# Optimization experiments

Measured on AMD Instinct MI355X. Metric: run time of the kernel, lower is better.

## Reference

```python
import jax, jax.numpy as jnp
import numpy as np

BLOCK_SIZE = 5
DROP_RATE = 0.5


def setup_inputs() -> dict:
    key = jax.random.key(0)
    k1, k2 = jax.random.split(key)
    B, C, H, W = 64, 128, 56, 56
    bs = BLOCK_SIZE
    x = jax.random.normal(k1, (B, C, H, W), dtype=jnp.float32)
    # uniform noise used to realize the Bernoulli(gamma) sample deterministically
    u = jax.random.uniform(k2, (B, C, H - bs + 1, W - bs + 1), dtype=jnp.float32)
    return {"x": x, "u": u, "num_batches_tracked": 1}


def reference(x, u, num_batches_tracked):
    bs = BLOCK_SIZE
    B, C, H, W = x.shape
    # keep-rate schedule (num_batches_tracked is a Python int => static)
    keep_rate = max(1.0 - DROP_RATE / 20000.0 * num_batches_tracked, 1.0 - DROP_RATE)
    gamma = (1.0 - keep_rate) / bs ** 2 * W ** 2 / (W - bs + 1) ** 2
    # Bernoulli(gamma) sample on the valid (H-bs+1, W-bs+1) grid
    mask = (u < gamma).astype(x.dtype)
    # The original scatters 1s at offsets 0..bs-1 around each sampled point into
    # a padded (H, W) mask. That is exactly a bs x bs max-pool dilation with
    # (bs-1, bs-1) zero padding on each spatial side, producing an (H, W) output.
    dilated = jax.lax.reduce_window(
        mask, 0.0, jax.lax.max,
        window_dimensions=(1, 1, bs, bs),
        window_strides=(1, 1, 1, 1),
        padding=((0, 0), (0, 0), (bs - 1, bs - 1), (bs - 1, bs - 1)),
    )
    block_mask = 1.0 - dilated  # (B, C, H, W)
    countM = block_mask.size
    count_ones = block_mask.sum()
    dind = (countM / count_ones) * block_mask
    return x * dind
```

## Files before the change

kernel.cpp:

```cpp
#include <hip/hip_runtime.h>

namespace {
constexpr int BSZ = 5;
constexpr int Bn = 64, Cn = 128, Hn = 56, Wn = 56;
constexpr int HU = Hn - BSZ + 1;
constexpr int WU = Wn - BSZ + 1;
constexpr long long NX = (long long)Bn * Cn * Hn * Wn;
constexpr long long NU = (long long)Bn * Cn * HU * WU;
constexpr int PLANE_U = HU * WU;
constexpr int PLANE_X = Hn * Wn;
constexpr int MAXH = 8192;

constexpr int NU4 = (int)(NU / 4);
constexpr int NX4 = (int)(NX / 4);
constexpr int SCAN_BLOCKS = NU4 / 256;
constexpr int MUL_BLOCKS = NX4 / 256;

struct Ctl {
  unsigned int nhits;
  unsigned int pad0;
  float scale;
  unsigned int hits[MAXH];
};
}

__global__ __launch_bounds__(256) void k_scan(const float4* __restrict__ u4,
                                              const int* __restrict__ nbt,
                                              Ctl* ctl) {
  double kr = 1.0 - 0.5 / 20000.0 * (double)nbt[0];
  if (kr < 0.5) kr = 0.5;
  double gd = (1.0 - kr) / (double)(BSZ * BSZ) * (double)(Wn * Wn) /
              (double)((Wn - BSZ + 1) * (Wn - BSZ + 1));
  const float g = (float)gd;

  const int i = blockIdx.x * 256 + threadIdx.x;
  float4 v = u4[i];
  if (v.x < g || v.y < g || v.z < g || v.w < g) {
    unsigned int base = (unsigned int)(4 * i);
    if (v.x < g) { unsigned int p = atomicAdd(&ctl->nhits, 1u); if (p < MAXH) ctl->hits[p] = base + 0u; }
    if (v.y < g) { unsigned int p = atomicAdd(&ctl->nhits, 1u); if (p < MAXH) ctl->hits[p] = base + 1u; }
    if (v.z < g) { unsigned int p = atomicAdd(&ctl->nhits, 1u); if (p < MAXH) ctl->hits[p] = base + 2u; }
    if (v.w < g) { unsigned int p = atomicAdd(&ctl->nhits, 1u); if (p < MAXH) ctl->hits[p] = base + 3u; }
  }
}

__global__ void k_count(Ctl* ctl) {
  __shared__ unsigned int s_total;
  if (threadIdx.x == 0) s_total = 0u;
  __syncthreads();
  const int n = (int)min(ctl->nhits, (unsigned int)MAXH);
  unsigned int local = 0;
  for (int t = threadIdx.x; t < n * 25; t += blockDim.x) {
    const int hi = t / 25;
    const int cell = t - hi * 25;
    const unsigned int e = ctl->hits[hi];
    const int plane = (int)(e / PLANE_U);
    const int rem = (int)(e - (unsigned int)plane * PLANE_U);
    const int i = rem / WU;
    const int j = rem - i * WU;
    const int hh = i + cell / 5;
    const int ww = j + cell % 5;
    bool covered = false;
    for (int p = 0; p < hi; ++p) {
      const unsigned int e2 = ctl->hits[p];
      const int pl2 = (int)(e2 / PLANE_U);
      if (pl2 != plane) continue;
      const int rem2 = (int)(e2 - (unsigned int)pl2 * PLANE_U);
      const int i2 = rem2 / WU;
      const int j2 = rem2 - i2 * WU;
      if (hh >= i2 && hh <= i2 + 4 && ww >= j2 && ww <= j2 + 4) { covered = true; break; }
    }
    if (!covered) local++;
  }
  if (local) atomicAdd(&s_total, local);
  __syncthreads();
  if (threadIdx.x == 0) {
    double count_ones = (double)NX - (double)s_total;
    ctl->scale = (float)((double)NX / count_ones);
  }
}

__global__ __launch_bounds__(256) void k_mul(const float4* __restrict__ x4,
                                             float4* __restrict__ o4,
                                             const Ctl* __restrict__ ctl) {
  const float s = ctl->scale;
  const int i = blockIdx.x * 256 + threadIdx.x;
  float4 v = x4[i];
  v.x *= s; v.y *= s; v.z *= s; v.w *= s;
  o4[i] = v;
}

__global__ void k_zero(float* __restrict__ out, const Ctl* __restrict__ ctl) {
  const int n = (int)min(ctl->nhits, (unsigned int)MAXH);
  const int total = n * 25;
  const int stride = gridDim.x * blockDim.x;
  for (int t = blockIdx.x * blockDim.x + threadIdx.x; t < total; t += stride) {
    const int hi = t / 25;
    const int cell = t - hi * 25;
    const unsigned int e = ctl->hits[hi];
    const int plane = (int)(e / PLANE_U);
    const int rem = (int)(e - (unsigned int)plane * PLANE_U);
    const int i = rem / WU;
    const int j = rem - i * WU;
    const int hh = i + cell / 5;
    const int ww = j + cell % 5;
    out[(long long)plane * PLANE_X + (long long)hh * Wn + ww] = 0.0f;
  }
}

extern "C" void kernel_launch(void* const* d_in, const int* in_sizes, int n_in,
                              void* d_out, int out_size, void* d_ws, size_t ws_size,
                              hipStream_t stream) {
  const float* x = (const float*)d_in[0];
  const float* u = (const float*)d_in[1];
  const int* nbt = (const int*)d_in[2];
  float* out = (float*)d_out;
  Ctl* ctl = (Ctl*)d_ws;

  hipMemsetAsync(ctl, 0, 8, stream);
  k_scan<<<SCAN_BLOCKS, 256, 0, stream>>>((const float4*)u, nbt, ctl);
  k_count<<<1, 256, 0, stream>>>(ctl);
  k_mul<<<MUL_BLOCKS, 256, 0, stream>>>((const float4*)x, (float4*)out, ctl);
  k_zero<<<16, 256, 0, stream>>>(out, ctl);
}
```

Measured before the change: 69.73 us.

## Fuse block zeroing into scale kernel and process four float4s per thread

Removes the separate k_zero launch by having k_mul check, per block, whether any recorded hit falls in its planes and, if so, zero the covered elements in registers before storing. Scan and mul kernels now handle four float4 per thread with a quarter of the blocks. This saves one kernel launch and the scattered zero writes. In exchange, every block scans the whole hit list, and blocks whose planes contain a hit then loop over all hits serially.

```diff
diff --git a/kernel.cpp b/kernel.cpp
--- a/kernel.cpp
+++ b/kernel.cpp
@@ -3,18 +3,15 @@
 namespace {
 constexpr int BSZ = 5;
 constexpr int Bn = 64, Cn = 128, Hn = 56, Wn = 56;
-constexpr int HU = Hn - BSZ + 1;
-constexpr int WU = Wn - BSZ + 1;
 constexpr long long NX = (long long)Bn * Cn * Hn * Wn;
-constexpr long long NU = (long long)Bn * Cn * HU * WU;
-constexpr int PLANE_U = HU * WU;
-constexpr int PLANE_X = Hn * Wn;
+constexpr long long NU = (long long)Bn * Cn * 52 * 52;
+constexpr int PLANE_U = 52 * 52;
+constexpr int PLANE_X4 = 784;
 constexpr int MAXH = 8192;
-
 constexpr int NU4 = (int)(NU / 4);
 constexpr int NX4 = (int)(NX / 4);
-constexpr int SCAN_BLOCKS = NU4 / 256;
-constexpr int MUL_BLOCKS = NX4 / 256;
+constexpr int SCAN_BLOCKS = NU4 / 1024;
+constexpr int MUL_BLOCKS  = NX4 / 1024;
 
 struct Ctl {
   unsigned int nhits;
@@ -22,26 +19,46 @@
   float scale;
   unsigned int hits[MAXH];
 };
+
+__device__ __forceinline__ void record_hits(float4 v, int idx4, float g, Ctl* ctl) {
+  if (v.x < g || v.y < g || v.z < g || v.w < g) {
+    unsigned int b = (unsigned int)(4 * idx4);
+    if (v.x < g) { unsigned int p = atomicAdd(&ctl->nhits, 1u); if (p < MAXH) ctl->hits[p] = b + 0u; }
+    if (v.y < g) { unsigned int p = atomicAdd(&ctl->nhits, 1u); if (p < MAXH) ctl->hits[p] = b + 1u; }
+    if (v.z < g) { unsigned int p = atomicAdd(&ctl->nhits, 1u); if (p < MAXH) ctl->hits[p] = b + 2u; }
+    if (v.w < g) { unsigned int p = atomicAdd(&ctl->nhits, 1u); if (p < MAXH) ctl->hits[p] = b + 3u; }
+  }
+}
+
+__device__ __forceinline__ void apply_hit(float4& a, int p, int row, int c0,
+                                          int hp, int hi, int hj) {
+  if (hp == p && row >= hi && row <= hi + 4) {
+    if (c0 + 0 >= hj && c0 + 0 <= hj + 4) a.x = 0.0f;
+    if (c0 + 1 >= hj && c0 + 1 <= hj + 4) a.y = 0.0f;
+    if (c0 + 2 >= hj && c0 + 2 <= hj + 4) a.z = 0.0f;
+    if (c0 + 3 >= hj && c0 + 3 <= hj + 4) a.w = 0.0f;
+  }
+}
 }
 
 __global__ __launch_bounds__(256) void k_scan(const float4* __restrict__ u4,
                                               const int* __restrict__ nbt,
-                                              Ctl* ctl) {
+                                              Ctl* __restrict__ ctl) {
   double kr = 1.0 - 0.5 / 20000.0 * (double)nbt[0];
   if (kr < 0.5) kr = 0.5;
   double gd = (1.0 - kr) / (double)(BSZ * BSZ) * (double)(Wn * Wn) /
               (double)((Wn - BSZ + 1) * (Wn - BSZ + 1));
   const float g = (float)gd;
 
-  const int i = blockIdx.x * 256 + threadIdx.x;
-  float4 v = u4[i];
-  if (v.x < g || v.y < g || v.z < g || v.w < g) {
-    unsigned int base = (unsigned int)(4 * i);
-    if (v.x < g) { unsigned int p = atomicAdd(&ctl->nhits, 1u); if (p < MAXH) ctl->hits[p] = base + 0u; }
-    if (v.y < g) { unsigned int p = atomicAdd(&ctl->nhits, 1u); if (p < MAXH) ctl->hits[p] = base + 1u; }
-    if (v.z < g) { unsigned int p = atomicAdd(&ctl->nhits, 1u); if (p < MAXH) ctl->hits[p] = base + 2u; }
-    if (v.w < g) { unsigned int p = atomicAdd(&ctl->nhits, 1u); if (p < MAXH) ctl->hits[p] = base + 3u; }
-  }
+  const int base = blockIdx.x * 1024 + threadIdx.x;
+  float4 v0 = u4[base];
+  float4 v1 = u4[base + 256];
+  float4 v2 = u4[base + 512];
+  float4 v3 = u4[base + 768];
+  record_hits(v0, base, g, ctl);
+  record_hits(v1, base + 256, g, ctl);
+  record_hits(v2, base + 512, g, ctl);
+  record_hits(v3, base + 768, g, ctl);
 }
 
 __global__ void k_count(Ctl* ctl) {
@@ -56,8 +73,8 @@
     const unsigned int e = ctl->hits[hi];
     const int plane = (int)(e / PLANE_U);
     const int rem = (int)(e - (unsigned int)plane * PLANE_U);
-    const int i = rem / WU;
-    const int j = rem - i * WU;
+    const int i = rem / 52;
+    const int j = rem - i * 52;
     const int hh = i + cell / 5;
     const int ww = j + cell % 5;
     bool covered = false;
@@ -66,8 +83,8 @@
       const int pl2 = (int)(e2 / PLANE_U);
       if (pl2 != plane) continue;
       const int rem2 = (int)(e2 - (unsigned int)pl2 * PLANE_U);
-      const int i2 = rem2 / WU;
-      const int j2 = rem2 - i2 * WU;
+      const int i2 = rem2 / 52;
+      const int j2 = rem2 - i2 * 52;
       if (hh >= i2 && hh <= i2 + 4 && ww >= j2 && ww <= j2 + 4) { covered = true; break; }
     }
     if (!covered) local++;
@@ -83,29 +100,56 @@
 __global__ __launch_bounds__(256) void k_mul(const float4* __restrict__ x4,
                                              float4* __restrict__ o4,
                                              const Ctl* __restrict__ ctl) {
+  const int blockStart = blockIdx.x * 1024;
+  const int base = blockStart + threadIdx.x;
+  float4 a0 = x4[base];
+  float4 a1 = x4[base + 256];
+  float4 a2 = x4[base + 512];
+  float4 a3 = x4[base + 768];
+
   const float s = ctl->scale;
-  const int i = blockIdx.x * 256 + threadIdx.x;
-  float4 v = x4[i];
-  v.x *= s; v.y *= s; v.z *= s; v.w *= s;
-  o4[i] = v;
-}
+  a0.x *= s; a0.y *= s; a0.z *= s; a0.w *= s;
+  a1.x *= s; a1.y *= s; a1.z *= s; a1.w *= s;
+  a2.x *= s; a2.y *= s; a2.z *= s; a2.w *= s;
+  a3.x *= s; a3.y *= s; a3.z *= s; a3.w *= s;
 
-__global__ void k_zero(float* __restrict__ out, const Ctl* __restrict__ ctl) {
   const int n = (int)min(ctl->nhits, (unsigned int)MAXH);
-  const int total = n * 25;
-  const int stride = gridDim.x * blockDim.x;
-  for (int t = blockIdx.x * blockDim.x + threadIdx.x; t < total; t += stride) {
-    const int hi = t / 25;
-    const int cell = t - hi * 25;
-    const unsigned int e = ctl->hits[hi];
-    const int plane = (int)(e / PLANE_U);
-    const int rem = (int)(e - (unsigned int)plane * PLANE_U);
-    const int i = rem / WU;
-    const int j = rem - i * WU;
-    const int hh = i + cell / 5;
-    const int ww = j + cell % 5;
-    out[(long long)plane * PLANE_X + (long long)hh * Wn + ww] = 0.0f;
+  const int pmin = blockStart / PLANE_X4;
+  const int pmax = (blockStart + 1023) / PLANE_X4;
+  bool any = false;
+  for (int h0 = 0; h0 < n; h0 += 64) {
+    const int h = h0 + (int)(threadIdx.x & 63);
+    bool mine = false;
+    if (h < n) {
+      const int hp = (int)(ctl->hits[h] / (unsigned int)PLANE_U);
+      mine = (hp >= pmin && hp <= pmax);
+    }
+    if (__any(mine)) { any = true; break; }
   }
+  if (any) {
+    const int f1 = base + 256, f2 = base + 512, f3 = base + 768;
+    const int p0 = base / PLANE_X4, p1 = f1 / PLANE_X4, p2 = f2 / PLANE_X4, p3 = f3 / PLANE_X4;
+    const int r0 = base - p0 * PLANE_X4, r1 = f1 - p1 * PLANE_X4,
+              r2 = f2 - p2 * PLANE_X4, r3 = f3 - p3 * PLANE_X4;
+    const int row0 = r0 / 14, row1 = r1 / 14, row2 = r2 / 14, row3 = r3 / 14;
+    const int c00 = (r0 - row0 * 14) * 4, c01 = (r1 - row1 * 14) * 4,
+              c02 = (r2 - row2 * 14) * 4, c03 = (r3 - row3 * 14) * 4;
+    for (int h = 0; h < n; ++h) {
+      const unsigned int e = ctl->hits[h];
+      const int hp = (int)(e / (unsigned int)PLANE_U);
+      const int rem = (int)(e - (unsigned int)hp * PLANE_U);
+      const int hi = rem / 52;
+      const int hj = rem - hi * 52;
+      apply_hit(a0, p0, row0, c00, hp, hi, hj);
+      apply_hit(a1, p1, row1, c01, hp, hi, hj);
+      apply_hit(a2, p2, row2, c02, hp, hi, hj);
+      apply_hit(a3, p3, row3, c03, hp, hi, hj);
+    }
+  }
+  o4[base] = a0;
+  o4[base + 256] = a1;
+  o4[base + 512] = a2;
+  o4[base + 768] = a3;
 }
 
 extern "C" void kernel_launch(void* const* d_in, const int* in_sizes, int n_in,
@@ -117,9 +161,8 @@
   float* out = (float*)d_out;
   Ctl* ctl = (Ctl*)d_ws;
 
-  hipMemsetAsync(ctl, 0, 8, stream);
+  hipMemsetAsync(&ctl->nhits, 0, sizeof(unsigned int), stream);
   k_scan<<<SCAN_BLOCKS, 256, 0, stream>>>((const float4*)u, nbt, ctl);
   k_count<<<1, 256, 0, stream>>>(ctl);
   k_mul<<<MUL_BLOCKS, 256, 0, stream>>>((const float4*)x, (float4*)out, ctl);
-  k_zero<<<16, 256, 0, stream>>>(out, ctl);
 }
```

Measured after the change: 70.11 us. Within noise of the previous version (+0.5%).

## Fuse scan, count, scale and mask into one persistent kernel with grid barrier

Applied to the files above, without the earlier changes.

Replaces the four separate kernels with one kernel where each block owns 8 planes: it scans its slice of u for hits into shared memory, counts uncovered cells locally, and adds that count to a global counter. It then prefetches part of x into registers, waits on a global atomic barrier for all blocks, computes the scale, and writes the output with masking applied inline. This removes extra launches and the separate zeroing pass. The barrier assumes all 1024 blocks are co-resident and falls back to a slow full rescan in every block if it times out.

```diff
diff --git a/kernel.cpp b/kernel.cpp
--- a/kernel.cpp
+++ b/kernel.cpp
@@ -1,125 +1,211 @@
 #include <hip/hip_runtime.h>
+
+typedef float f32x4 __attribute__((ext_vector_type(4)));
 
 namespace {
 constexpr int BSZ = 5;
-constexpr int Bn = 64, Cn = 128, Hn = 56, Wn = 56;
-constexpr int HU = Hn - BSZ + 1;
-constexpr int WU = Wn - BSZ + 1;
-constexpr long long NX = (long long)Bn * Cn * Hn * Wn;
-constexpr long long NU = (long long)Bn * Cn * HU * WU;
-constexpr int PLANE_U = HU * WU;
-constexpr int PLANE_X = Hn * Wn;
-constexpr int MAXH = 8192;
-
-constexpr int NU4 = (int)(NU / 4);
-constexpr int NX4 = (int)(NX / 4);
-constexpr int SCAN_BLOCKS = NU4 / 256;
-constexpr int MUL_BLOCKS = NX4 / 256;
-
-struct Ctl {
-  unsigned int nhits;
-  unsigned int pad0;
-  float scale;
-  unsigned int hits[MAXH];
-};
-}
-
-__global__ __launch_bounds__(256) void k_scan(const float4* __restrict__ u4,
+constexpr int Wn = 56;
+constexpr long long NX = 25690112;
+constexpr int NBLK = 1024;
+constexpr int T = 512;
+constexpr int PPB = 8;
+constexpr int U_PLANE = 2704;
+constexpr int UB = PPB * U_PLANE / 4;
+constexpr int XB = PPB * 3136 / 4;
+constexpr int PF = 10;
+constexpr int MAXL = 64;
+constexpr int NU4 = 5537792;
+
+__device__ __forceinline__ void mask_f4(f32x4& a, int k, const unsigned short* hits, int n) {
+  const int pl = k / 784;
+  const int rem4 = k - pl * 784;
+  const int row = rem4 / 14;
+  const int c0 = (rem4 - row * 14) * 4;
+  for (int h = 0; h < n; ++h) {
+    const int lin = hits[h];
+    const int hp = lin / U_PLANE;
+    if (hp != pl) continue;
+    const int hrem = lin - hp * U_PLANE;
+    const int hi = hrem / 52;
+    const int hj = hrem - hi * 52;
+    if (row >= hi && row <= hi + 4) {
+      if (c0 + 0 >= hj && c0 + 0 <= hj + 4) a.x = 0.0f;
+      if (c0 + 1 >= hj && c0 + 1 <= hj + 4) a.y = 0.0f;
+      if (c0 + 2 >= hj && c0 + 2 <= hj + 4) a.z = 0.0f;
+      if (c0 + 3 >= hj && c0 + 3 <= hj + 4) a.w = 0.0f;
+    }
+  }
+}
+}
+
+__global__ __launch_bounds__(T, 8) void k_all(const f32x4* __restrict__ u4,
+                                              const f32x4* __restrict__ x4,
+                                              f32x4* __restrict__ o4,
                                               const int* __restrict__ nbt,
-                                              Ctl* ctl) {
+                                              unsigned int* __restrict__ ws) {
+  const int tid = threadIdx.x;
+  const int blk = blockIdx.x;
+
   double kr = 1.0 - 0.5 / 20000.0 * (double)nbt[0];
   if (kr < 0.5) kr = 0.5;
   double gd = (1.0 - kr) / (double)(BSZ * BSZ) * (double)(Wn * Wn) /
               (double)((Wn - BSZ + 1) * (Wn - BSZ + 1));
   const float g = (float)gd;
 
-  const int i = blockIdx.x * 256 + threadIdx.x;
-  float4 v = u4[i];
-  if (v.x < g || v.y < g || v.z < g || v.w < g) {
-    unsigned int base = (unsigned int)(4 * i);
-    if (v.x < g) { unsigned int p = atomicAdd(&ctl->nhits, 1u); if (p < MAXH) ctl->hits[p] = base + 0u; }
-    if (v.y < g) { unsigned int p = atomicAdd(&ctl->nhits, 1u); if (p < MAXH) ctl->hits[p] = base + 1u; }
-    if (v.z < g) { unsigned int p = atomicAdd(&ctl->nhits, 1u); if (p < MAXH) ctl->hits[p] = base + 2u; }
-    if (v.w < g) { unsigned int p = atomicAdd(&ctl->nhits, 1u); if (p < MAXH) ctl->hits[p] = base + 3u; }
-  }
-}
-
-__global__ void k_count(Ctl* ctl) {
-  __shared__ unsigned int s_total;
-  if (threadIdx.x == 0) s_total = 0u;
-  __syncthreads();
-  const int n = (int)min(ctl->nhits, (unsigned int)MAXH);
-  unsigned int local = 0;
-  for (int t = threadIdx.x; t < n * 25; t += blockDim.x) {
-    const int hi = t / 25;
-    const int cell = t - hi * 25;
-    const unsigned int e = ctl->hits[hi];
-    const int plane = (int)(e / PLANE_U);
-    const int rem = (int)(e - (unsigned int)plane * PLANE_U);
-    const int i = rem / WU;
-    const int j = rem - i * WU;
-    const int hh = i + cell / 5;
-    const int ww = j + cell % 5;
-    bool covered = false;
-    for (int p = 0; p < hi; ++p) {
-      const unsigned int e2 = ctl->hits[p];
-      const int pl2 = (int)(e2 / PLANE_U);
-      if (pl2 != plane) continue;
-      const int rem2 = (int)(e2 - (unsigned int)pl2 * PLANE_U);
-      const int i2 = rem2 / WU;
-      const int j2 = rem2 - i2 * WU;
-      if (hh >= i2 && hh <= i2 + 4 && ww >= j2 && ww <= j2 + 4) { covered = true; break; }
-    }
-    if (!covered) local++;
-  }
-  if (local) atomicAdd(&s_total, local);
-  __syncthreads();
-  if (threadIdx.x == 0) {
-    double count_ones = (double)NX - (double)s_total;
-    ctl->scale = (float)((double)NX / count_ones);
-  }
-}
-
-__global__ __launch_bounds__(256) void k_mul(const float4* __restrict__ x4,
-                                             float4* __restrict__ o4,
-                                             const Ctl* __restrict__ ctl) {
-  const float s = ctl->scale;
-  const int i = blockIdx.x * 256 + threadIdx.x;
-  float4 v = x4[i];
-  v.x *= s; v.y *= s; v.z *= s; v.w *= s;
-  o4[i] = v;
-}
-
-__global__ void k_zero(float* __restrict__ out, const Ctl* __restrict__ ctl) {
-  const int n = (int)min(ctl->nhits, (unsigned int)MAXH);
-  const int total = n * 25;
-  const int stride = gridDim.x * blockDim.x;
-  for (int t = blockIdx.x * blockDim.x + threadIdx.x; t < total; t += stride) {
-    const int hi = t / 25;
-    const int cell = t - hi * 25;
-    const unsigned int e = ctl->hits[hi];
-    const int plane = (int)(e / PLANE_U);
-    const int rem = (int)(e - (unsigned int)plane * PLANE_U);
-    const int i = rem / WU;
-    const int j = rem - i * WU;
-    const int hh = i + cell / 5;
-    const int ww = j + cell % 5;
-    out[(long long)plane * PLANE_X + (long long)hh * Wn + ww] = 0.0f;
+  __shared__ unsigned short s_hits[MAXL];
+  __shared__ unsigned int s_n, s_cnt, s_gcount, s_gn;
+  __shared__ int s_to;
+  __shared__ unsigned int s_ghits[256];
+  if (tid == 0) { s_n = 0u; s_cnt = 0u; }
+  __syncthreads();
+
+  const int ubase = blk * UB;
+  for (int k = tid; k < UB; k += T) {
+    f32x4 v = __builtin_nontemporal_load(u4 + ubase + k);
+    if (v.x < g || v.y < g || v.z < g || v.w < g) {
+      const unsigned int b4 = 4u * (unsigned int)k;
+      if (v.x < g) { unsigned p = atomicAdd(&s_n, 1u); if (p < MAXL) s_hits[p] = (unsigned short)(b4 + 0u); }
+      if (v.y < g) { unsigned p = atomicAdd(&s_n, 1u); if (p < MAXL) s_hits[p] = (unsigned short)(b4 + 1u); }
+      if (v.z < g) { unsigned p = atomicAdd(&s_n, 1u); if (p < MAXL) s_hits[p] = (unsigned short)(b4 + 2u); }
+      if (v.w < g) { unsigned p = atomicAdd(&s_n, 1u); if (p < MAXL) s_hits[p] = (unsigned short)(b4 + 3u); }
+    }
+  }
+  __syncthreads();
+
+  const int n = (int)min(s_n, (unsigned)MAXL);
+  for (int t = tid; t < n * 25; t += T) {
+    const int hidx = t / 25, cell = t - hidx * 25;
+    const int lin = s_hits[hidx];
+    const int pl = lin / U_PLANE;
+    const int rem = lin - pl * U_PLANE;
+    const int i = rem / 52, j = rem - (rem / 52) * 52;
+    const int hh = i + cell / 5, ww = j + cell % 5;
+    bool cov = false;
+    for (int p = 0; p < hidx; ++p) {
+      const int lin2 = s_hits[p];
+      const int pl2 = lin2 / U_PLANE;
+      if (pl2 != pl) continue;
+      const int rem2 = lin2 - pl2 * U_PLANE;
+      const int i2 = rem2 / 52, j2 = rem2 - (rem2 / 52) * 52;
+      if (hh >= i2 && hh <= i2 + 4 && ww >= j2 && ww <= j2 + 4) { cov = true; break; }
+    }
+    if (!cov) atomicAdd(&s_cnt, 1u);
+  }
+  __syncthreads();
+  if (tid == 0 && s_cnt)
+    __hip_atomic_fetch_add(&ws[1], s_cnt, __ATOMIC_RELAXED, __HIP_MEMORY_SCOPE_AGENT);
+
+  const long long xb = (long long)blk * XB;
+  f32x4 r0 = __builtin_nontemporal_load(x4 + xb + tid + 0 * T);
+  f32x4 r1 = __builtin_nontemporal_load(x4 + xb + tid + 1 * T);
+  f32x4 r2 = __builtin_nontemporal_load(x4 + xb + tid + 2 * T);
+  f32x4 r3 = __builtin_nontemporal_load(x4 + xb + tid + 3 * T);
+  f32x4 r4 = __builtin_nontemporal_load(x4 + xb + tid + 4 * T);
+  f32x4 r5 = __builtin_nontemporal_load(x4 + xb + tid + 5 * T);
+  f32x4 r6 = __builtin_nontemporal_load(x4 + xb + tid + 6 * T);
+  f32x4 r7 = __builtin_nontemporal_load(x4 + xb + tid + 7 * T);
+  f32x4 r8 = __builtin_nontemporal_load(x4 + xb + tid + 8 * T);
+  f32x4 r9 = __builtin_nontemporal_load(x4 + xb + tid + 9 * T);
+  asm volatile("" : "+v"(r0), "+v"(r1), "+v"(r2), "+v"(r3), "+v"(r4),
+                    "+v"(r5), "+v"(r6), "+v"(r7), "+v"(r8), "+v"(r9));
+
+  __syncthreads();
+
+  if (tid == 0) {
+    s_to = 0;
+    __hip_atomic_fetch_add(&ws[0], 1u, __ATOMIC_RELEASE, __HIP_MEMORY_SCOPE_AGENT);
+    int it = 0;
+    while (__hip_atomic_load(&ws[0], __ATOMIC_ACQUIRE, __HIP_MEMORY_SCOPE_AGENT) <
+           (unsigned)NBLK) {
+      __builtin_amdgcn_s_sleep(2);
+      if (++it > (1 << 16)) { s_to = 1; break; }
+    }
+    s_gcount = __hip_atomic_load(&ws[1], __ATOMIC_RELAXED, __HIP_MEMORY_SCOPE_AGENT);
+  }
+  __syncthreads();
+
+  if (s_to) {
+    if (tid == 0) { s_gn = 0u; s_cnt = 0u; }
+    __syncthreads();
+    for (int k = tid; k < NU4; k += T) {
+      f32x4 v = u4[k];
+      const unsigned int b4 = 4u * (unsigned int)k;
+      if (v.x < g) { unsigned p = atomicAdd(&s_gn, 1u); if (p < 256u) s_ghits[p] = b4 + 0u; }
+      if (v.y < g) { unsigned p = atomicAdd(&s_gn, 1u); if (p < 256u) s_ghits[p] = b4 + 1u; }
+      if (v.z < g) { unsigned p = atomicAdd(&s_gn, 1u); if (p < 256u) s_ghits[p] = b4 + 2u; }
+      if (v.w < g) { unsigned p = atomicAdd(&s_gn, 1u); if (p < 256u) s_ghits[p] = b4 + 3u; }
+    }
+    __syncthreads();
+    const int gn = (int)min(s_gn, 256u);
+    for (int t = tid; t < gn * 25; t += T) {
+      const int hidx = t / 25, cell = t - hidx * 25;
+      const unsigned int lin = s_ghits[hidx];
+      const int pl = (int)(lin / (unsigned)U_PLANE);
+      const int rem = (int)(lin - (unsigned)pl * U_PLANE);
+      const int i = rem / 52, j = rem - (rem / 52) * 52;
+      const int hh = i + cell / 5, ww = j + cell % 5;
+      bool cov = false;
+      for (int p = 0; p < hidx; ++p) {
+        const unsigned int lin2 = s_ghits[p];
+        const int pl2 = (int)(lin2 / (unsigned)U_PLANE);
+        if (pl2 != pl) continue;
+        const int rem2 = (int)(lin2 - (unsigned)pl2 * U_PLANE);
+        const int i2 = rem2 / 52, j2 = rem2 - (rem2 / 52) * 52;
+        if (hh >= i2 && hh <= i2 + 4 && ww >= j2 && ww <= j2 + 4) { cov = true; break; }
+      }
+      if (!cov) atomicAdd(&s_cnt, 1u);
+    }
+    __syncthreads();
+    if (tid == 0) s_gcount = s_cnt;
+    __syncthreads();
+  }
+
+  const double count_ones = (double)NX - (double)s_gcount;
+  const float s = (float)((double)NX / count_ones);
+
+  const int n2 = (int)min(s_n, (unsigned)MAXL);
+  r0 *= s; r1 *= s; r2 *= s; r3 *= s; r4 *= s;
+  r5 *= s; r6 *= s; r7 *= s; r8 *= s; r9 *= s;
+  if (n2) {
+    mask_f4(r0, tid + 0 * T, s_hits, n2);
+    mask_f4(r1, tid + 1 * T, s_hits, n2);
+    mask_f4(r2, tid + 2 * T, s_hits, n2);
+    mask_f4(r3, tid + 3 * T, s_hits, n2);
+    mask_f4(r4, tid + 4 * T, s_hits, n2);
+    mask_f4(r5, tid + 5 * T, s_hits, n2);
+    mask_f4(r6, tid + 6 * T, s_hits, n2);
+    mask_f4(r7, tid + 7 * T, s_hits, n2);
+    mask_f4(r8, tid + 8 * T, s_hits, n2);
+    mask_f4(r9, tid + 9 * T, s_hits, n2);
+  }
+  __builtin_nontemporal_store(r0, o4 + xb + tid + 0 * T);
+  __builtin_nontemporal_store(r1, o4 + xb + tid + 1 * T);
+  __builtin_nontemporal_store(r2, o4 + xb + tid + 2 * T);
+  __builtin_nontemporal_store(r3, o4 + xb + tid + 3 * T);
+  __builtin_nontemporal_store(r4, o4 + xb + tid + 4 * T);
+  __builtin_nontemporal_store(r5, o4 + xb + tid + 5 * T);
+  __builtin_nontemporal_store(r6, o4 + xb + tid + 6 * T);
+  __builtin_nontemporal_store(r7, o4 + xb + tid + 7 * T);
+  __builtin_nontemporal_store(r8, o4 + xb + tid + 8 * T);
+  __builtin_nontemporal_store(r9, o4 + xb + tid + 9 * T);
+
+  for (int k = PF * T + tid; k < XB; k += T) {
+    f32x4 a = __builtin_nontemporal_load(x4 + xb + k);
+    a *= s;
+    if (n2) mask_f4(a, k, s_hits, n2);
+    __builtin_nontemporal_store(a, o4 + xb + k);
   }
 }
 
 extern "C" void kernel_launch(void* const* d_in, const int* in_sizes, int n_in,
                               void* d_out, int out_size, void* d_ws, size_t ws_size,
                               hipStream_t stream) {
-  const float* x = (const float*)d_in[0];
-  const float* u = (const float*)d_in[1];
+  const f32x4* x = (const f32x4*)d_in[0];
+  const f32x4* u = (const f32x4*)d_in[1];
   const int* nbt = (const int*)d_in[2];
-  float* out = (float*)d_out;
-  Ctl* ctl = (Ctl*)d_ws;
-
-  hipMemsetAsync(ctl, 0, 8, stream);
-  k_scan<<<SCAN_BLOCKS, 256, 0, stream>>>((const float4*)u, nbt, ctl);
-  k_count<<<1, 256, 0, stream>>>(ctl);
-  k_mul<<<MUL_BLOCKS, 256, 0, stream>>>((const float4*)x, (float4*)out, ctl);
-  k_zero<<<16, 256, 0, stream>>>(out, ctl);
-}
+  f32x4* out = (f32x4*)d_out;
+  unsigned int* ws = (unsigned int*)d_ws;
+
+  hipMemsetAsync(ws, 0, 8, stream);
+  k_all<<<NBLK, T, 0, stream>>>(u, x, out, nbt, ws);
+}
```

New measurement: 210.3 us. 202% more time.
